# Optimization experiments

Hardware: AMD Instinct MI355X
Metric: run time of the kernel (lower is better)

## Reference

```python
import jax, jax.numpy as jnp
import numpy as np

DIM = 256; HEADS = 8; WH = 7; WW = 7; TOPK = 4; BATCH = 8; NUM_WIN = 64
N_TOK = WH * WW
HEAD_DIM = DIM // HEADS
SCALE = HEAD_DIM ** -0.5


def _rel_pos_index():
    # identical to the torch buffer construction (meshgrid indexing='ij')
    ch = np.arange(WH); cw = np.arange(WW)
    coords = np.stack(np.meshgrid(ch, cw, indexing='ij'))          # (2, Wh, Ww)
    cf = coords.reshape(2, -1)                                     # (2, N)
    rel = cf[:, :, None] - cf[:, None, :]                          # (2, N, N)
    rel = rel.transpose(1, 2, 0).copy()                            # (N, N, 2)
    rel[:, :, 0] += WH - 1
    rel[:, :, 1] += WW - 1
    rel[:, :, 0] *= 2 * WW - 1
    return rel.sum(-1)                                             # (N, N) int


def setup_inputs() -> dict:
    key = jax.random.key(0)
    ks = jax.random.split(key, 5)
    B_ = BATCH * NUM_WIN
    x = jax.random.normal(ks[0], (B_, N_TOK, DIM), jnp.float32)
    w_qkv = jax.random.normal(ks[1], (DIM, 3 * DIM), jnp.float32) * (DIM ** -0.5)
    b_qkv = jnp.zeros((3 * DIM,), jnp.float32)
    rel_bias_table = 0.02 * jax.random.normal(ks[2], ((2 * WH - 1) * (2 * WW - 1), HEADS), jnp.float32)
    w_proj = jax.random.normal(ks[3], (DIM, DIM), jnp.float32) * (DIM ** -0.5)
    b_proj = jnp.zeros((DIM,), jnp.float32)
    return {"x": x, "w_qkv": w_qkv, "b_qkv": b_qkv, "rel_bias_table": rel_bias_table,
            "w_proj": w_proj, "b_proj": b_proj, "batch": BATCH}


def reference(x, w_qkv, b_qkv, rel_bias_table, w_proj, b_proj, batch):
    B_, N, C = x.shape
    H, d, tk = HEADS, HEAD_DIM, TOPK
    nw = B_ // batch  # num_windows (window index is MAJOR in the leading dim)
    qkv = (x @ w_qkv + b_qkv).reshape(B_, N, 3, H, d).transpose(2, 0, 3, 1, 4)
    q, k, v = qkv[0], qkv[1], qkv[2]  # each (B_, H, N, d)

    # ---- MoE gate (faithful: key_gate_weight repeats the SAME per-window mean-k
    # across the n axis, so all gate columns are equal; the identity column is set
    # to +inf). The top-k values/indices do not affect the output because the
    # subsequent torch.gather(dim=0) is index-independent (see below).
    mean_k = jnp.mean(k, axis=2, keepdims=True)                       # (B_, H, 1, d)
    gate = jnp.einsum('bhlc,bhnc->bhln', q, jnp.broadcast_to(mean_k, (B_, H, nw, d)))
    gate = gate.reshape(nw, batch, H, N, nw)
    eye = jnp.eye(nw, dtype=bool)[:, None, None, None, :]
    gate = jnp.where(eye, jnp.inf, gate)
    _gate_vals, _gate_idx = jax.lax.top_k(gate, tk)                   # unused downstream

    # ---- gathered K/V. In the torch code, k is broadcast over a 'rep' axis (dim 0)
    # and then gathered along that SAME axis, so out[r,...,t] = k_windows[t,...]:
    # every query window attends to windows 0..topk-1. We materialize exactly that.
    k_rs = k.reshape(nw, batch, H, N, d)
    v_rs = v.reshape(nw, batch, H, N, d)
    # layout after torch permute(0,5,1,2,3,4).reshape(topk*B_, H, N, d): (rep, t, batch) major->minor
    k_g = jnp.broadcast_to(k_rs[:tk][None], (nw, tk, batch, H, N, d)).reshape(tk * B_, H, N, d)
    v_g = jnp.broadcast_to(v_rs[:tk][None], (nw, tk, batch, H, N, d)).reshape(tk * B_, H, N, d)

    q_rep = jnp.repeat(q, tk, axis=0) * SCALE                         # (tk*B_, H, N, d)

    attn = jnp.einsum('bhqd,bhkd->bhqk', q_rep, k_g)                  # (tk*B_, H, N, N)
    rel_idx = _rel_pos_index()
    bias = rel_bias_table[rel_idx.reshape(-1)].reshape(N, N, H).transpose(2, 0, 1)
    attn = jax.nn.softmax(attn + bias[None], axis=-1)

    out = jnp.einsum('bhqk,bhkd->bhqd', attn, v_g)                    # (tk*B_, H, N, d)
    out = out.reshape(tk, B_, H, N, d).mean(axis=0)                   # literal torch reshape
    out = out.transpose(0, 2, 1, 3).reshape(B_, N, C)
    return out @ w_proj + b_proj
```

## Files before the change

kernel.cpp:

```cpp
#include <hip/hip_runtime.h>
#include <hip/hip_bf16.h>
#include <math.h>


#define N_TOK   49
#define DIMC    256
#define HEADS   8
#define HEAD_D  32
#define BWIN    512
#define NKV     32
#define MROWS   (BWIN * N_TOK)
#define KVROWS  (NKV * N_TOK)
#define SCALE_L2 (0.17677669529663687f * 1.4426950408889634f)
#define LOG2E    1.4426950408889634f

__device__ __forceinline__ void gemm_tile_128(
    const float* __restrict__ A, int M,
    const float* __restrict__ W, int ldw, int wcol0,
    const float* __restrict__ bias,
    float* __restrict__ C, int ldc,
    int mt, int nt, float* As )
{
    const int tid = threadIdx.x;
    const int tr  = tid >> 4;
    const int tc  = tid & 15;
    const int R0  = mt * 128;
    const int C0  = nt * 128;
    const int wc0 = wcol0 + C0 + tc * 8;

    float acc[8][8];
    #pragma unroll
    for (int j = 0; j < 8; ++j) {
        float bj = bias[wc0 + j];
        #pragma unroll
        for (int i = 0; i < 8; ++i) acc[i][j] = bj;
    }

    for (int kc = 0; kc < 8; ++kc) {
        if (kc) __syncthreads();
        #pragma unroll
        for (int it = 0; it < 4; ++it) {
            int flat = it * 256 + tid;
            int row  = flat >> 3;
            int q8   = flat & 7;
            int gr   = R0 + row; if (gr > M - 1) gr = M - 1;
            float4 v = *(const float4*)(A + (size_t)gr * 256 + kc * 32 + q8 * 4);
            int q8s  = q8 ^ ((row >> 3) & 7);
            *(float4*)(As + row * 32 + q8s * 4) = v;
        }
        __syncthreads();

        #pragma unroll
        for (int kk4 = 0; kk4 < 8; ++kk4) {
            float a[8][4];
            const int cg = (kk4 ^ (tr & 7)) << 2;
            #pragma unroll
            for (int i = 0; i < 8; ++i) {
                float4 t = *(const float4*)(As + (tr * 8 + i) * 32 + cg);
                a[i][0] = t.x; a[i][1] = t.y; a[i][2] = t.z; a[i][3] = t.w;
            }
            #pragma unroll
            for (int dk = 0; dk < 4; ++dk) {
                const float* wp = W + (size_t)(kc * 32 + kk4 * 4 + dk) * ldw + wc0;
                float4 w0 = *(const float4*)(wp);
                float4 w1 = *(const float4*)(wp + 4);
                float wv[8] = {w0.x, w0.y, w0.z, w0.w, w1.x, w1.y, w1.z, w1.w};
                #pragma unroll
                for (int i = 0; i < 8; ++i) {
                    float av = a[i][dk];
                    #pragma unroll
                    for (int j = 0; j < 8; ++j)
                        acc[i][j] = fmaf(av, wv[j], acc[i][j]);
                }
            }
        }
    }

    #pragma unroll
    for (int i = 0; i < 8; ++i) {
        int gr = R0 + tr * 8 + i;
        if (gr < M) {
            float* cp = C + (size_t)gr * ldc + C0 + tc * 8;
            float4 s0 = {acc[i][0], acc[i][1], acc[i][2], acc[i][3]};
            float4 s1 = {acc[i][4], acc[i][5], acc[i][6], acc[i][7]};
            *(float4*)(cp)     = s0;
            *(float4*)(cp + 4) = s1;
        }
    }
}

__global__ __launch_bounds__(256) void k_gemm_qkv(
    const float* __restrict__ x, const float* __restrict__ w,
    const float* __restrict__ b, float* __restrict__ qbuf,
    float* __restrict__ kvbuf)
{
    __shared__ float As[128 * 32];
    int bx = blockIdx.x;
    if (bx < 392) {
        gemm_tile_128(x, MROWS, w, 768, 0,   b, qbuf,  256, bx >> 1, bx & 1, As);
    } else {
        int b2 = bx - 392;
        gemm_tile_128(x, KVROWS, w, 768, 256, b, kvbuf, 512, b2 >> 2, b2 & 3, As);
    }
}

__global__ __launch_bounds__(256) void k_gemm_proj(
    const float* __restrict__ ob, const float* __restrict__ w,
    const float* __restrict__ b, float* __restrict__ out)
{
    __shared__ float As[128 * 32];
    gemm_tile_128(ob, MROWS, w, 256, 0, b, out, 256, blockIdx.x >> 1, blockIdx.x & 1, As);
}

__global__ __launch_bounds__(256, 4) void k_attn(
    const float* __restrict__ qbuf,
    const float* __restrict__ kvbuf,
    const float* __restrict__ table,
    float* __restrict__ obuf)
{
    __shared__ float Ks[49 * 32];
    __shared__ float Vs[49 * 32];
    __shared__ float Bs[49 * 49];

    const int kv  = blockIdx.x;
    const int h   = blockIdx.y;
    const int wg  = blockIdx.z;
    const int tid = threadIdx.x;

    const float* kvb = kvbuf + (size_t)(kv * 49) * 512 + h * 32;
    for (int idx = tid; idx < 392; idx += 256) {
        int row = idx >> 3, q4 = idx & 7;
        const float* src = kvb + row * 512 + q4 * 4;
        ((float4*)Ks)[idx] = *(const float4*)src;
        ((float4*)Vs)[idx] = *(const float4*)(src + 256);
    }
    for (int idx = tid; idx < 2401; idx += 256) {
        int r = idx / 49, j = idx - r * 49;
        int rh = r / 7, rw = r - rh * 7;
        int jh = j / 7, jw = j - jh * 7;
        int t = ((rh - jh + 6) * 13 + (rw - jw + 6)) * HEADS + h;
        Bs[idx] = table[t] * LOG2E;
    }
    __syncthreads();

    const int lane = tid & 63;
    const int wi   = tid >> 6;
    const int w    = wg * 4 + wi;
    const int m    = kv + 32 * w;
    const int r    = lane < 49 ? lane : 48;
    const float* brow = Bs + r * 49;

    float o_tot[32];
    #pragma unroll
    for (int d = 0; d < 32; ++d) o_tot[d] = 0.f;

    for (int tt = 0; tt < 4; ++tt) {
        const int qidx = tt * 128 + (m >> 2);
        const float* qp = qbuf + ((size_t)qidx * 49 + r) * 256 + h * 32;
        float q[32];
        #pragma unroll
        for (int d4 = 0; d4 < 8; ++d4) {
            float4 t4 = *(const float4*)(qp + d4 * 4);
            q[d4*4+0] = t4.x * SCALE_L2; q[d4*4+1] = t4.y * SCALE_L2;
            q[d4*4+2] = t4.z * SCALE_L2; q[d4*4+3] = t4.w * SCALE_L2;
        }

        float o_tt[32];
        #pragma unroll
        for (int d = 0; d < 32; ++d) o_tt[d] = 0.f;
        float sum = 0.f;

        #pragma unroll 7
        for (int j = 0; j < 49; ++j) {
            const float* kp = Ks + j * 32;
            float a0 = 0.f, a1 = 0.f, a2 = 0.f, a3 = 0.f;
            #pragma unroll
            for (int d4 = 0; d4 < 8; ++d4) {
                float4 k4 = *(const float4*)(kp + d4 * 4);
                a0 = fmaf(q[d4*4+0], k4.x, a0);
                a1 = fmaf(q[d4*4+1], k4.y, a1);
                a2 = fmaf(q[d4*4+2], k4.z, a2);
                a3 = fmaf(q[d4*4+3], k4.w, a3);
            }
            const float e = exp2f((a0 + a1) + (a2 + a3) + brow[j]);
            sum += e;

            const float* vp = Vs + j * 32;
            #pragma unroll
            for (int d4 = 0; d4 < 8; ++d4) {
                float4 v4 = *(const float4*)(vp + d4 * 4);
                o_tt[d4*4+0] = fmaf(e, v4.x, o_tt[d4*4+0]);
                o_tt[d4*4+1] = fmaf(e, v4.y, o_tt[d4*4+1]);
                o_tt[d4*4+2] = fmaf(e, v4.z, o_tt[d4*4+2]);
                o_tt[d4*4+3] = fmaf(e, v4.w, o_tt[d4*4+3]);
            }
        }

        const float inv = 1.0f / sum;
        #pragma unroll
        for (int d = 0; d < 32; ++d) o_tot[d] = fmaf(o_tt[d], inv, o_tot[d]);
    }

    if (lane < 49) {
        float* op = obuf + ((size_t)m * 49 + lane) * 256 + h * 32;
        #pragma unroll
        for (int d4 = 0; d4 < 8; ++d4) {
            float4 t = {o_tot[d4*4+0] * 0.25f, o_tot[d4*4+1] * 0.25f,
                        o_tot[d4*4+2] * 0.25f, o_tot[d4*4+3] * 0.25f};
            *(float4*)(op + d4 * 4) = t;
        }
    }
}

extern "C" void kernel_launch(void* const* d_in, const int* in_sizes, int n_in,
                              void* d_out, int out_size, void* d_ws, size_t ws_size,
                              hipStream_t stream)
{
    const float* x      = (const float*)d_in[0];
    const float* w_qkv  = (const float*)d_in[1];
    const float* b_qkv  = (const float*)d_in[2];
    const float* table  = (const float*)d_in[3];
    const float* w_proj = (const float*)d_in[4];
    const float* b_proj = (const float*)d_in[5];
    float* out = (float*)d_out;

    float* qbuf  = (float*)d_ws;
    float* kvbuf = qbuf + (size_t)MROWS * 256;
    float* obuf  = kvbuf + (size_t)KVROWS * 512;

    k_gemm_qkv<<<444, 256, 0, stream>>>(x, w_qkv, b_qkv, qbuf, kvbuf);
    k_attn<<<dim3(32, 8, 4), 256, 0, stream>>>(qbuf, kvbuf, table, obuf);
    k_gemm_proj<<<392, 256, 0, stream>>>(obuf, w_proj, b_proj, out);
}
```

Baseline: 341.1 us.

## Switch projection GEMMs to bf16 MFMA with bf16 intermediates

Adds a prep kernel that converts x to bf16 and transposes both weight matrices to bf16. The QKV and output-projection GEMMs are rewritten to use bf16 MFMA 16x16x32 instructions, with tiles loaded into shared memory through global_load_lds. Q and the attention output are now stored as bf16, which halves their memory traffic. The aim is to replace the scalar fp32 FMA GEMMs with matrix cores, at the cost of lower precision and an extra conversion pass over x every call.

```diff
diff --git a/kernel.cpp b/kernel.cpp
--- a/kernel.cpp
+++ b/kernel.cpp
@@ -4,123 +4,162 @@
 
 
 #define N_TOK   49
-#define DIMC    256
 #define HEADS   8
-#define HEAD_D  32
-#define BWIN    512
-#define NKV     32
-#define MROWS   (BWIN * N_TOK)
-#define KVROWS  (NKV * N_TOK)
+#define MROWS   25088
+#define KVROWS  1568
 #define SCALE_L2 (0.17677669529663687f * 1.4426950408889634f)
 #define LOG2E    1.4426950408889634f
 
-__device__ __forceinline__ void gemm_tile_128(
-    const float* __restrict__ A, int M,
-    const float* __restrict__ W, int ldw, int wcol0,
+using bf16x8 = __attribute__((ext_vector_type(8))) short;
+using f32x4  = __attribute__((ext_vector_type(4))) float;
+
+__device__ __forceinline__ ushort f2b(float f) {
+    __hip_bfloat16 h = __float2bfloat16(f);
+    ushort u; __builtin_memcpy(&u, &h, 2); return u;
+}
+
+__global__ __launch_bounds__(256) void k_prep(
+    const float* __restrict__ x, const float* __restrict__ wq,
+    const float* __restrict__ wp, ushort* __restrict__ xb,
+    ushort* __restrict__ wqT, ushort* __restrict__ wpT)
+{
+    int bx = blockIdx.x, tid = threadIdx.x;
+    if (bx < 6272) {
+        int i = bx * 256 + tid;
+        float4 v = ((const float4*)x)[i];
+        ushort4 o = {f2b(v.x), f2b(v.y), f2b(v.z), f2b(v.w)};
+        *(ushort4*)(xb + 4 * (size_t)i) = o;
+    } else if (bx < 7040) {
+        int j = (bx - 6272) * 256 + tid;
+        int n = j >> 8, k = j & 255;
+        wqT[j] = f2b(wq[(size_t)k * 768 + n]);
+    } else {
+        int j = (bx - 7040) * 256 + tid;
+        int n = j >> 8, k = j & 255;
+        wpT[j] = f2b(wp[(size_t)k * 256 + n]);
+    }
+}
+
+template<int MODE>
+__device__ __forceinline__ void mfma_tile(
+    const ushort* __restrict__ Ab, int M,
+    const ushort* __restrict__ WT,
     const float* __restrict__ bias,
-    float* __restrict__ C, int ldc,
-    int mt, int nt, float* As )
+    void* __restrict__ Cout,
+    int R0, int NT0, ushort* As, ushort* Bs)
 {
     const int tid = threadIdx.x;
-    const int tr  = tid >> 4;
-    const int tc  = tid & 15;
-    const int R0  = mt * 128;
-    const int C0  = nt * 128;
-    const int wc0 = wcol0 + C0 + tc * 8;
-
-    float acc[8][8];
+    const int wid = tid >> 6, lane = tid & 63;
+    const int wr = wid >> 1, wc = wid & 1;
+    const int l15 = lane & 15, kg = lane >> 4;
+
+    f32x4 acc[4][4];
     #pragma unroll
-    for (int j = 0; j < 8; ++j) {
-        float bj = bias[wc0 + j];
-        #pragma unroll
-        for (int i = 0; i < 8; ++i) acc[i][j] = bj;
-    }
-
-    for (int kc = 0; kc < 8; ++kc) {
+    for (int mi = 0; mi < 4; ++mi)
+        #pragma unroll
+        for (int ni = 0; ni < 4; ++ni)
+            acc[mi][ni] = (f32x4){0.f, 0.f, 0.f, 0.f};
+
+    for (int kc = 0; kc < 4; ++kc) {
         if (kc) __syncthreads();
         #pragma unroll
         for (int it = 0; it < 4; ++it) {
-            int flat = it * 256 + tid;
-            int row  = flat >> 3;
-            int q8   = flat & 7;
-            int gr   = R0 + row; if (gr > M - 1) gr = M - 1;
-            float4 v = *(const float4*)(A + (size_t)gr * 256 + kc * 32 + q8 * 4);
-            int q8s  = q8 ^ ((row >> 3) & 7);
-            *(float4*)(As + row * 32 + q8s * 4) = v;
+            int f    = it * 256 + tid;
+            int row  = f >> 3, slot = f & 7;
+            int sl   = slot ^ (row & 7);
+            char* dst = (char*)As + (size_t)it * 4096 + wid * 1024;
+            int ga   = R0 + row; if (ga > M - 1) ga = M - 1;
+            __builtin_amdgcn_global_load_lds(
+                (const void*)(Ab + (size_t)ga * 256 + kc * 64 + sl * 8),
+                (void*)dst, 16, 0, 0);
+            char* dstB = (char*)Bs + (size_t)it * 4096 + wid * 1024;
+            __builtin_amdgcn_global_load_lds(
+                (const void*)(WT + (size_t)(NT0 + row) * 256 + kc * 64 + sl * 8),
+                (void*)dstB, 16, 0, 0);
         }
         __syncthreads();
 
         #pragma unroll
-        for (int kk4 = 0; kk4 < 8; ++kk4) {
-            float a[8][4];
-            const int cg = (kk4 ^ (tr & 7)) << 2;
-            #pragma unroll
-            for (int i = 0; i < 8; ++i) {
-                float4 t = *(const float4*)(As + (tr * 8 + i) * 32 + cg);
-                a[i][0] = t.x; a[i][1] = t.y; a[i][2] = t.z; a[i][3] = t.w;
-            }
-            #pragma unroll
-            for (int dk = 0; dk < 4; ++dk) {
-                const float* wp = W + (size_t)(kc * 32 + kk4 * 4 + dk) * ldw + wc0;
-                float4 w0 = *(const float4*)(wp);
-                float4 w1 = *(const float4*)(wp + 4);
-                float wv[8] = {w0.x, w0.y, w0.z, w0.w, w1.x, w1.y, w1.z, w1.w};
+        for (int ks = 0; ks < 2; ++ks) {
+            bf16x8 af[4], bfr[4];
+            #pragma unroll
+            for (int t = 0; t < 4; ++t) {
+                int arow = wr * 64 + t * 16 + l15;
+                int aslt = (ks * 4 + kg) ^ (arow & 7);
+                af[t]  = *(const bf16x8*)((const char*)As + arow * 128 + aslt * 16);
+                int brow = wc * 64 + t * 16 + l15;
+                int bslt = (ks * 4 + kg) ^ (brow & 7);
+                bfr[t] = *(const bf16x8*)((const char*)Bs + brow * 128 + bslt * 16);
+            }
+            #pragma unroll
+            for (int mi = 0; mi < 4; ++mi)
                 #pragma unroll
-                for (int i = 0; i < 8; ++i) {
-                    float av = a[i][dk];
-                    #pragma unroll
-                    for (int j = 0; j < 8; ++j)
-                        acc[i][j] = fmaf(av, wv[j], acc[i][j]);
+                for (int ni = 0; ni < 4; ++ni)
+                    acc[mi][ni] = __builtin_amdgcn_mfma_f32_16x16x32_bf16(
+                        af[mi], bfr[ni], acc[mi][ni], 0, 0, 0);
+        }
+    }
+
+    #pragma unroll
+    for (int ni = 0; ni < 4; ++ni) {
+        int colW = NT0 + wc * 64 + ni * 16 + l15;
+        float bv = bias[colW];
+        #pragma unroll
+        for (int mi = 0; mi < 4; ++mi) {
+            #pragma unroll
+            for (int r = 0; r < 4; ++r) {
+                float v = acc[mi][ni][r] + bv;
+                int grow = R0 + wr * 64 + mi * 16 + kg * 4 + r;
+                if (MODE == 0) {
+                    ((ushort*)Cout)[(size_t)grow * 256 + colW] = f2b(v);
+                } else if (MODE == 1) {
+                    if (grow < M)
+                        ((float*)Cout)[(size_t)grow * 512 + (colW - 256)] = v;
+                } else {
+                    ((float*)Cout)[(size_t)grow * 256 + colW] = v;
                 }
             }
         }
     }
-
-    #pragma unroll
-    for (int i = 0; i < 8; ++i) {
-        int gr = R0 + tr * 8 + i;
-        if (gr < M) {
-            float* cp = C + (size_t)gr * ldc + C0 + tc * 8;
-            float4 s0 = {acc[i][0], acc[i][1], acc[i][2], acc[i][3]};
-            float4 s1 = {acc[i][4], acc[i][5], acc[i][6], acc[i][7]};
-            *(float4*)(cp)     = s0;
-            *(float4*)(cp + 4) = s1;
-        }
-    }
 }
 
 __global__ __launch_bounds__(256) void k_gemm_qkv(
-    const float* __restrict__ x, const float* __restrict__ w,
-    const float* __restrict__ b, float* __restrict__ qbuf,
-    float* __restrict__ kvbuf)
-{
-    __shared__ float As[128 * 32];
+    const ushort* __restrict__ xb, const ushort* __restrict__ wqT,
+    const float* __restrict__ b, ushort* __restrict__ qb,
+    float* __restrict__ kv)
+{
+    __shared__ ushort As[128 * 64];
+    __shared__ ushort Bs[128 * 64];
     int bx = blockIdx.x;
     if (bx < 392) {
-        gemm_tile_128(x, MROWS, w, 768, 0,   b, qbuf,  256, bx >> 1, bx & 1, As);
+        mfma_tile<0>(xb, MROWS, wqT, b, qb, (bx >> 1) * 128, (bx & 1) * 128, As, Bs);
     } else {
         int b2 = bx - 392;
-        gemm_tile_128(x, KVROWS, w, 768, 256, b, kvbuf, 512, b2 >> 2, b2 & 3, As);
+        mfma_tile<1>(xb, KVROWS, wqT, b, kv, (b2 >> 2) * 128, 256 + (b2 & 3) * 128, As, Bs);
     }
 }
 
 __global__ __launch_bounds__(256) void k_gemm_proj(
-    const float* __restrict__ ob, const float* __restrict__ w,
+    const ushort* __restrict__ ob, const ushort* __restrict__ wpT,
     const float* __restrict__ b, float* __restrict__ out)
 {
-    __shared__ float As[128 * 32];
-    gemm_tile_128(ob, MROWS, w, 256, 0, b, out, 256, blockIdx.x >> 1, blockIdx.x & 1, As);
-}
-
-__global__ __launch_bounds__(256, 4) void k_attn(
-    const float* __restrict__ qbuf,
+    __shared__ ushort As[128 * 64];
+    __shared__ ushort Bs[128 * 64];
+    mfma_tile<2>(ob, MROWS, wpT, b, out, (blockIdx.x >> 1) * 128,
+                 (blockIdx.x & 1) * 128, As, Bs);
+}
+
+__global__ __launch_bounds__(256)
+__attribute__((amdgpu_waves_per_eu(4, 4)))
+void k_attn(
+    const ushort* __restrict__ qb,
     const float* __restrict__ kvbuf,
     const float* __restrict__ table,
-    float* __restrict__ obuf)
+    ushort* __restrict__ obuf)
 {
     __shared__ float Ks[49 * 32];
     __shared__ float Vs[49 * 32];
-    __shared__ float Bs[49 * 49];
+    __shared__ float Bsh[49 * 49];
 
     const int kv  = blockIdx.x;
     const int h   = blockIdx.y;
@@ -139,7 +178,7 @@
         int rh = r / 7, rw = r - rh * 7;
         int jh = j / 7, jw = j - jh * 7;
         int t = ((rh - jh + 6) * 13 + (rw - jw + 6)) * HEADS + h;
-        Bs[idx] = table[t] * LOG2E;
+        Bsh[idx] = table[t] * LOG2E;
     }
     __syncthreads();
 
@@ -148,7 +187,7 @@
     const int w    = wg * 4 + wi;
     const int m    = kv + 32 * w;
     const int r    = lane < 49 ? lane : 48;
-    const float* brow = Bs + r * 49;
+    const float* brow = Bsh + r * 49;
 
     float o_tot[32];
     #pragma unroll
@@ -156,13 +195,17 @@
 
     for (int tt = 0; tt < 4; ++tt) {
         const int qidx = tt * 128 + (m >> 2);
-        const float* qp = qbuf + ((size_t)qidx * 49 + r) * 256 + h * 32;
+        const ushort* qp = qb + ((size_t)qidx * 49 + r) * 256 + h * 32;
         float q[32];
         #pragma unroll
-        for (int d4 = 0; d4 < 8; ++d4) {
-            float4 t4 = *(const float4*)(qp + d4 * 4);
-            q[d4*4+0] = t4.x * SCALE_L2; q[d4*4+1] = t4.y * SCALE_L2;
-            q[d4*4+2] = t4.z * SCALE_L2; q[d4*4+3] = t4.w * SCALE_L2;
+        for (int g = 0; g < 4; ++g) {
+            uint4 u = *(const uint4*)(qp + g * 8);
+            uint uu[4] = {u.x, u.y, u.z, u.w};
+            #pragma unroll
+            for (int p = 0; p < 4; ++p) {
+                q[g*8 + 2*p]     = __uint_as_float(uu[p] << 16) * SCALE_L2;
+                q[g*8 + 2*p + 1] = __uint_as_float(uu[p] & 0xffff0000u) * SCALE_L2;
+            }
         }
 
         float o_tt[32];
@@ -202,12 +245,18 @@
     }
 
     if (lane < 49) {
-        float* op = obuf + ((size_t)m * 49 + lane) * 256 + h * 32;
-        #pragma unroll
-        for (int d4 = 0; d4 < 8; ++d4) {
-            float4 t = {o_tot[d4*4+0] * 0.25f, o_tot[d4*4+1] * 0.25f,
-                        o_tot[d4*4+2] * 0.25f, o_tot[d4*4+3] * 0.25f};
-            *(float4*)(op + d4 * 4) = t;
+        ushort* op = obuf + ((size_t)m * 49 + lane) * 256 + h * 32;
+        #pragma unroll
+        for (int g = 0; g < 4; ++g) {
+            uint4 pkd;
+            uint* pu = (uint*)&pkd;
+            #pragma unroll
+            for (int p = 0; p < 4; ++p) {
+                uint lo = f2b(o_tot[g*8 + 2*p]     * 0.25f);
+                uint hi = f2b(o_tot[g*8 + 2*p + 1] * 0.25f);
+                pu[p] = lo | (hi << 16);
+            }
+            *(uint4*)(op + g * 8) = pkd;
         }
     }
 }
@@ -224,11 +273,16 @@
     const float* b_proj = (const float*)d_in[5];
     float* out = (float*)d_out;
 
-    float* qbuf  = (float*)d_ws;
-    float* kvbuf = qbuf + (size_t)MROWS * 256;
-    float* obuf  = kvbuf + (size_t)KVROWS * 512;
-
-    k_gemm_qkv<<<444, 256, 0, stream>>>(x, w_qkv, b_qkv, qbuf, kvbuf);
-    k_attn<<<dim3(32, 8, 4), 256, 0, stream>>>(qbuf, kvbuf, table, obuf);
-    k_gemm_proj<<<392, 256, 0, stream>>>(obuf, w_proj, b_proj, out);
-}
+    char* p = (char*)d_ws;
+    ushort* qb  = (ushort*)p;                 p += (size_t)MROWS * 256 * 2;
+    float*  kvb = (float*)p;                  p += (size_t)KVROWS * 512 * 4;
+    ushort* ob  = (ushort*)p;                 p += (size_t)MROWS * 256 * 2;
+    ushort* xb  = (ushort*)p;                 p += (size_t)MROWS * 256 * 2;
+    ushort* wqT = (ushort*)p;                 p += (size_t)768 * 256 * 2;
+    ushort* wpT = (ushort*)p;
+
+    k_prep<<<7296, 256, 0, stream>>>(x, w_qkv, w_proj, xb, wqT, wpT);
+    k_gemm_qkv<<<444, 256, 0, stream>>>(xb, wqT, b_qkv, qb, kvb);
+    k_attn<<<dim3(32, 8, 4), 256, 0, stream>>>(qb, kvb, table, ob);
+    k_gemm_proj<<<392, 256, 0, stream>>>(ob, wpT, b_proj, out);
+}
```

New measurement: 275.6 us. 1.24x faster.
